# Kernel optimization log

Hardware: AMD Instinct MI355X
Metric: run time of the kernel (lower is better)

## Reference

```python
import jax, jax.numpy as jnp
import numpy as np
from jax import lax

B, N, C, H, M = 256, 2048, 128, 64, 50
NMS_THRESH = 2.0  # forward() calls target_nms(..., 2)
LN_EPS = 1e-5


def setup_inputs() -> dict:
    key = jax.random.key(0)
    ks = jax.random.split(key, 32)
    w = lambda k, shape: jax.random.normal(k, shape, jnp.float32) * 0.02
    gt_idx = jax.random.randint(ks[2], (B,), 0, N)
    inp = {
        "feat_in": jax.random.normal(ks[0], (B, 1, C), jnp.float32),
        "tar_candidate": jax.random.normal(ks[1], (B, N, 2), jnp.float32) * 10.0,
        "mask": jnp.zeros((B, N, 1), jnp.float32),
        "candidate_gt": jax.nn.one_hot(gt_idx, N, dtype=jnp.float32),
        "offset_gt": jax.random.normal(ks[3], (B, 2), jnp.float32),
    }
    Din = C + 2
    # prob_mlp params
    inp.update(p_w1=w(ks[4], (Din, H)), p_b1=jnp.zeros((H,)), p_g1=jnp.ones((H,)), p_be1=jnp.zeros((H,)),
               p_w2=w(ks[5], (H, H)), p_b2=jnp.zeros((H,)), p_g2=jnp.ones((H,)), p_be2=jnp.zeros((H,)),
               p_w3=w(ks[6], (H, 1)), p_b3=jnp.zeros((1,)))
    # offset_mlp params
    inp.update(o_w1=w(ks[7], (Din, H)), o_b1=jnp.zeros((H,)), o_g1=jnp.ones((H,)), o_be1=jnp.zeros((H,)),
               o_w2=w(ks[8], (H, H)), o_g2=jnp.ones((H,)), o_b2=jnp.zeros((H,)), o_be2=jnp.zeros((H,)),
               o_w3=w(ks[9], (H, 2)), o_b3=jnp.zeros((2,)))
    return inp


def _ln(x, g, b):
    mu = jnp.mean(x, axis=-1, keepdims=True)
    var = jnp.mean((x - mu) ** 2, axis=-1, keepdims=True)
    return (x - mu) * lax.rsqrt(var + LN_EPS) * g + b


def _mlp(x, w1, b1, g1, be1, w2, b2, g2, be2, w3, b3):
    h = jax.nn.relu(_ln(x @ w1 + b1, g1, be1))
    h = jax.nn.relu(_ln(h @ w2 + b2, g2, be2))
    return h @ w3 + b3


def _target_nms(targets, threshold):
    # targets: [B, 50, 2] -> [B, 6, 2], sequential dedup per batch row
    def per_batch(t):
        sel0 = t[:6]

        def step(carry, i):
            sel, cnt = carry
            d = jnp.sum((sel - t[i]) ** 2, axis=1)            # [6]
            valid = jnp.arange(6) < cnt
            close = jnp.any((d < threshold) & valid)
            accept = jnp.logical_and(~close, cnt < 6)
            sel = sel.at[cnt].set(jnp.where(accept, t[i], sel[cnt]))
            cnt = cnt + accept.astype(jnp.int32)
            return (sel, cnt), None

        (sel, _), _ = lax.scan(step, (sel0, jnp.int32(1)), jnp.arange(1, M))
        return sel

    return jax.vmap(per_batch)(targets)


def _forward(feat_in, tar_candidate, mask, candidate_gt, offset_gt,
             p_w1, p_b1, p_g1, p_be1, p_w2, p_b2, p_g2, p_be2, p_w3, p_b3,
             o_w1, o_b1, o_g1, o_be1, o_w2, o_b2, o_g2, o_be2, o_w3, o_b3):
    b, n, _ = tar_candidate.shape
    feat_rep = jnp.concatenate(
        [jnp.broadcast_to(feat_in, (b, n, feat_in.shape[-1])), tar_candidate], axis=2)  # [B,N,C+2]

    prob_tensor = _mlp(feat_rep, p_w1, p_b1, p_g1, p_be1, p_w2, p_b2, p_g2, p_be2, p_w3, p_b3)
    prob_tensor = prob_tensor + mask
    tar_candit_prob = jax.nn.softmax(prob_tensor, axis=1)[..., 0]                      # [B,N]

    tar_offset = _mlp(feat_rep, o_w1, o_b1, o_g1, o_be1, o_w2, o_b2, o_g2, o_be2, o_w3, o_b3)  # [B,N,2]

    _, idx = lax.top_k(tar_candit_prob, M)                                             # [B,50]
    idx3 = jnp.repeat(idx[:, :, None], 2, axis=2)
    tar_sel = jnp.take_along_axis(tar_candidate, idx3, axis=1) + jnp.take_along_axis(tar_offset, idx3, axis=1)
    tar_sel = _target_nms(tar_sel, NMS_THRESH)                                         # [B,6,2]

    # loss: BCE(prob, gt) + smooth_l1(offset[gt], offset_gt); gt is one-hot per row
    p = tar_candit_prob
    bce = -jnp.mean(candidate_gt * jnp.clip(jnp.log(p), -100.0)
                    + (1.0 - candidate_gt) * jnp.clip(jnp.log1p(-p), -100.0))
    gt_idx = jnp.argmax(candidate_gt, axis=1)                                          # [B]
    off_pred = tar_offset[jnp.arange(b), gt_idx]                                       # [B,2]
    d = off_pred - offset_gt
    ad = jnp.abs(d)
    sl1 = jnp.mean(jnp.where(ad < 1.0, 0.5 * d * d, ad - 0.5))
    loss = bce + sl1
    return tar_sel, loss


def reference(feat_in, tar_candidate, mask, candidate_gt, offset_gt,
              p_w1, p_b1, p_g1, p_be1, p_w2, p_b2, p_g2, p_be2, p_w3, p_b3,
              o_w1, o_b1, o_g1, o_be1, o_w2, o_b2, o_g2, o_be2, o_w3, o_b3):
    return _forward(feat_in, tar_candidate, mask, candidate_gt, offset_gt,
                    p_w1, p_b1, p_g1, p_be1, p_w2, p_b2, p_g2, p_be2, p_w3, p_b3,
                    o_w1, o_b1, o_g1, o_be1, o_w2, o_b2, o_g2, o_be2, o_w3, o_b3)
```

## Files before the change

### kernel.cpp

```cpp
#include <hip/hip_runtime.h>
#include <hip/hip_bf16.h>
#include <math.h>

#define Bb 256
#define Nn 2048
#define Cc 128
#define Hh 64
#define Mm 50

__global__ __launch_bounds__(128) void k_base(const float* __restrict__ feat,
                                              const float* __restrict__ p_w1,
                                              const float* __restrict__ p_b1,
                                              const float* __restrict__ o_w1,
                                              const float* __restrict__ o_b1,
                                              float* __restrict__ basep,
                                              float* __restrict__ baseo) {
    int b = blockIdx.x, tid = threadIdx.x;
    int k = tid & 63;
    bool lo = tid < 64;
    const float* w1 = lo ? p_w1 : o_w1;
    const float* b1 = lo ? p_b1 : o_b1;
    float* dst = lo ? basep : baseo;
    const float* f = feat + b * Cc;
    float s = b1[k];
    #pragma unroll 8
    for (int c = 0; c < Cc; ++c) s = fmaf(f[c], w1[c * Hh + k], s);
    dst[b * Hh + k] = s;
}

__global__ __launch_bounds__(256, 1) void k_mlp_p(
    const float* __restrict__ cand, const float* __restrict__ basep,
    const float* __restrict__ p_w1, const float* __restrict__ p_g1, const float* __restrict__ p_be1,
    const float* __restrict__ p_w2, const float* __restrict__ p_b2,
    const float* __restrict__ p_g2, const float* __restrict__ p_be2,
    const float* __restrict__ p_w3, const float* __restrict__ p_b3,
    float* __restrict__ logits)
{
    int tid = threadIdx.x;
    int b = blockIdx.x >> 3;
    int n = ((blockIdx.x & 7) << 8) + tid;
    long row = (long)b * Nn + n;
    float cx = cand[row * 2 + 0];
    float cy = cand[row * 2 + 1];
    const float* basev = basep + b * Hh;
    const float* u = p_w1 + 128 * Hh;
    const float* v = p_w1 + 129 * Hh;

    float a[Hh];
    float sum = 0.f, sq = 0.f;
    #pragma unroll
    for (int j = 0; j < Hh; ++j) {
        float t = fmaf(cy, v[j], fmaf(cx, u[j], basev[j]));
        a[j] = t;
        sum += t;
        sq = fmaf(t, t, sq);
    }
    float mu = sum * (1.f / Hh);
    float rstd = rsqrtf(sq * (1.f / Hh) - mu * mu + 1e-5f);
    #pragma unroll
    for (int j = 0; j < Hh; ++j)
        a[j] = fmaxf(fmaf((a[j] - mu) * rstd, p_g1[j], p_be1[j]), 0.f);

    float h[Hh];
    #pragma unroll
    for (int i = 0; i < Hh; ++i) h[i] = 0.f;
    #pragma unroll
    for (int j = 0; j < Hh; ++j) {
        float av = a[j];
        const float* w2r = p_w2 + j * Hh;
        #pragma unroll
        for (int i = 0; i < Hh; ++i) h[i] = fmaf(av, w2r[i], h[i]);
    }
    float sum2 = 0.f, sq2 = 0.f;
    #pragma unroll
    for (int i = 0; i < Hh; ++i) {
        float hv = h[i] + p_b2[i];
        h[i] = hv;
        sum2 += hv;
        sq2 = fmaf(hv, hv, sq2);
    }
    float mu2 = sum2 * (1.f / Hh);
    float rstd2 = rsqrtf(sq2 * (1.f / Hh) - mu2 * mu2 + 1e-5f);

    float lg = p_b3[0];
    #pragma unroll
    for (int i = 0; i < Hh; ++i) {
        float aa = fmaxf(fmaf((h[i] - mu2) * rstd2, p_g2[i], p_be2[i]), 0.f);
        lg = fmaf(aa, p_w3[i], lg);
    }
    logits[row] = lg;
}

__global__ __launch_bounds__(256) void k_post(
    const float* __restrict__ logits, const float* __restrict__ mask,
    const float* __restrict__ gt,
    float* __restrict__ bce_part, int* __restrict__ selidx_g, int* __restrict__ gidx_g)
{
    __shared__ float vals[Nn];
    __shared__ float redf[4];
    __shared__ float wvv[4]; __shared__ int wvi[4];
    __shared__ int   gidx_sh;
    __shared__ int   wini_sh;
    __shared__ int   selidx[Mm];

    int b = blockIdx.x, tid = threadIdx.x;
    int wave = tid >> 6, lane = tid & 63;
    const float* lg = logits + (long)b * Nn;
    const float* mk = mask + (long)b * Nn;

    float xv[8];
    float mx = -1e30f;
    #pragma unroll
    for (int k = 0; k < 8; ++k) {
        int n = tid + k * 256;
        xv[k] = lg[n] + mk[n];
        mx = fmaxf(mx, xv[k]);
    }
    #pragma unroll
    for (int m = 1; m < 64; m <<= 1) mx = fmaxf(mx, __shfl_xor(mx, m));
    if (lane == 0) redf[wave] = mx;
    __syncthreads();
    float m = fmaxf(fmaxf(redf[0], redf[1]), fmaxf(redf[2], redf[3]));
    __syncthreads();

    float ev[8]; float es = 0.f;
    #pragma unroll
    for (int k = 0; k < 8; ++k) { ev[k] = expf(xv[k] - m); es += ev[k]; }
    #pragma unroll
    for (int mm = 1; mm < 64; mm <<= 1) es += __shfl_xor(es, mm);
    if (lane == 0) redf[wave] = es;
    __syncthreads();
    float invZ = 1.f / (((redf[0] + redf[1]) + redf[2]) + redf[3]);

    const float* g = gt + (long)b * Nn;
    float bs = 0.f;
    #pragma unroll
    for (int k = 0; k < 8; ++k) {
        int n = tid + k * 256;
        float pv = ev[k] * invZ;
        vals[n] = pv;
        float gv = g[n];
        float lp = fmaxf(logf(pv), -100.f);
        float l1p = fmaxf(log1pf(-pv), -100.f);
        bs += gv * lp + (1.f - gv) * l1p;
        if (gv > 0.5f) gidx_sh = n;
    }
    #pragma unroll
    for (int mm = 1; mm < 64; mm <<= 1) bs += __shfl_xor(bs, mm);
    if (lane == 0) redf[wave] = bs;
    __syncthreads();
    if (tid == 0) {
        bce_part[b] = ((redf[0] + redf[1]) + redf[2]) + redf[3];
        gidx_g[b] = gidx_sh;
    }

    float bv = -1.f; int bi = 0x7fffffff;
    #pragma unroll
    for (int k = 0; k < 8; ++k) {
        int n = tid + k * 256;
        float v = vals[n];
        if (v > bv) { bv = v; bi = n; }
    }
    for (int it = 0; it < Mm; ++it) {
        float rv = bv; int ri = bi;
        #pragma unroll
        for (int mm = 1; mm < 64; mm <<= 1) {
            float v2 = __shfl_xor(rv, mm); int i2 = __shfl_xor(ri, mm);
            if (v2 > rv || (v2 == rv && i2 < ri)) { rv = v2; ri = i2; }
        }
        if (lane == 0) { wvv[wave] = rv; wvi[wave] = ri; }
        __syncthreads();
        if (tid == 0) {
            float wv = wvv[0]; int wi = wvi[0];
            #pragma unroll
            for (int k = 1; k < 4; ++k) {
                if (wvv[k] > wv || (wvv[k] == wv && wvi[k] < wi)) { wv = wvv[k]; wi = wvi[k]; }
            }
            wini_sh = wi;
            selidx[it] = wi;
        }
        __syncthreads();
        int wi = wini_sh;
        if ((wi & 255) == tid) {
            vals[wi] = -1.f;
            bv = -1.f; bi = 0x7fffffff;
            #pragma unroll
            for (int k = 0; k < 8; ++k) {
                int n = tid + k * 256;
                float v = vals[n];
                if (v > bv) { bv = v; bi = n; }
            }
        }
    }
    if (tid < Mm) selidx_g[b * Mm + tid] = selidx[tid];
}

__device__ __forceinline__ void off_mlp_row(
    long row, const float* __restrict__ cand, const float* __restrict__ basev,
    const float* __restrict__ o_w1, const float* __restrict__ o_g1, const float* __restrict__ o_be1,
    const float* __restrict__ o_w2, const float* __restrict__ o_b2,
    const float* __restrict__ o_g2, const float* __restrict__ o_be2,
    const float* __restrict__ o_w3, const float* __restrict__ o_b3,
    float& o0, float& o1)
{
    float cx = cand[row * 2 + 0];
    float cy = cand[row * 2 + 1];
    const float* u = o_w1 + 128 * Hh;
    const float* v = o_w1 + 129 * Hh;
    float a[Hh];
    float sum = 0.f, sq = 0.f;
    #pragma unroll
    for (int j = 0; j < Hh; ++j) {
        float t = fmaf(cy, v[j], fmaf(cx, u[j], basev[j]));
        a[j] = t;
        sum += t;
        sq = fmaf(t, t, sq);
    }
    float mu = sum * (1.f / Hh);
    float rstd = rsqrtf(sq * (1.f / Hh) - mu * mu + 1e-5f);
    #pragma unroll
    for (int j = 0; j < Hh; ++j)
        a[j] = fmaxf(fmaf((a[j] - mu) * rstd, o_g1[j], o_be1[j]), 0.f);
    float h[Hh];
    #pragma unroll
    for (int i = 0; i < Hh; ++i) h[i] = 0.f;
    #pragma unroll
    for (int j = 0; j < Hh; ++j) {
        float av = a[j];
        const float* w2r = o_w2 + j * Hh;
        #pragma unroll
        for (int i = 0; i < Hh; ++i) h[i] = fmaf(av, w2r[i], h[i]);
    }
    float sum2 = 0.f, sq2 = 0.f;
    #pragma unroll
    for (int i = 0; i < Hh; ++i) {
        float hv = h[i] + o_b2[i];
        h[i] = hv;
        sum2 += hv;
        sq2 = fmaf(hv, hv, sq2);
    }
    float mu2 = sum2 * (1.f / Hh);
    float rstd2 = rsqrtf(sq2 * (1.f / Hh) - mu2 * mu2 + 1e-5f);
    o0 = o_b3[0]; o1 = o_b3[1];
    #pragma unroll
    for (int i = 0; i < Hh; ++i) {
        float aa = fmaxf(fmaf((h[i] - mu2) * rstd2, o_g2[i], o_be2[i]), 0.f);
        o0 = fmaf(aa, o_w3[i * 2 + 0], o0);
        o1 = fmaf(aa, o_w3[i * 2 + 1], o1);
    }
}

__global__ __launch_bounds__(64, 1) void k_off(
    const float* __restrict__ cand, const float* __restrict__ baseo,
    const int* __restrict__ selidx_g, const int* __restrict__ gidx_g,
    const float* __restrict__ off_gt,
    const float* __restrict__ o_w1, const float* __restrict__ o_g1, const float* __restrict__ o_be1,
    const float* __restrict__ o_w2, const float* __restrict__ o_b2,
    const float* __restrict__ o_g2, const float* __restrict__ o_be2,
    const float* __restrict__ o_w3, const float* __restrict__ o_b3,
    float* __restrict__ out, float* __restrict__ sl1_part)
{
    __shared__ float tx[Mm], ty[Mm];
    int b = blockIdx.x, tid = threadIdx.x;
    const float* basev = baseo + b * Hh;

    int idx;
    if (tid < Mm)        idx = selidx_g[b * Mm + tid];
    else if (tid == Mm)  idx = gidx_g[b];
    else                 idx = 0;
    long row = (long)b * Nn + idx;

    float o0, o1;
    off_mlp_row(row, cand, basev, o_w1, o_g1, o_be1, o_w2, o_b2, o_g2, o_be2, o_w3, o_b3, o0, o1);

    if (tid < Mm) {
        tx[tid] = cand[row * 2 + 0] + o0;
        ty[tid] = cand[row * 2 + 1] + o1;
    } else if (tid == Mm) {
        float s1 = 0.f;
        float d0 = o0 - off_gt[b * 2 + 0];
        float ad0 = fabsf(d0);
        s1 += (ad0 < 1.f) ? 0.5f * d0 * d0 : ad0 - 0.5f;
        float d1 = o1 - off_gt[b * 2 + 1];
        float ad1 = fabsf(d1);
        s1 += (ad1 < 1.f) ? 0.5f * d1 * d1 : ad1 - 0.5f;
        sl1_part[b] = s1;
    }
    __syncthreads();
    if (tid == 0) {
        float sx[6], sy[6];
        #pragma unroll
        for (int k = 0; k < 6; ++k) { sx[k] = tx[k]; sy[k] = ty[k]; }
        int cnt = 1;
        for (int i = 1; i < Mm; ++i) {
            bool close = false;
            #pragma unroll
            for (int k = 0; k < 6; ++k) {
                float dx = sx[k] - tx[i], dy = sy[k] - ty[i];
                close = close || ((k < cnt) && (dx * dx + dy * dy < 2.0f));
            }
            if (!close && cnt < 6) { sx[cnt] = tx[i]; sy[cnt] = ty[i]; cnt++; }
        }
        #pragma unroll
        for (int k = 0; k < 6; ++k) {
            out[(b * 6 + k) * 2 + 0] = sx[k];
            out[(b * 6 + k) * 2 + 1] = sy[k];
        }
    }
}

__global__ __launch_bounds__(256) void k_loss(const float* __restrict__ bce_part,
                                              const float* __restrict__ sl1_part,
                                              float* __restrict__ out) {
    __shared__ float redb[4], reds[4];
    int tid = threadIdx.x, wave = tid >> 6, lane = tid & 63;
    float sb = bce_part[tid];
    float ss = sl1_part[tid];
    #pragma unroll
    for (int mm = 1; mm < 64; mm <<= 1) { sb += __shfl_xor(sb, mm); ss += __shfl_xor(ss, mm); }
    if (lane == 0) { redb[wave] = sb; reds[wave] = ss; }
    __syncthreads();
    if (tid == 0) {
        float tb = ((redb[0] + redb[1]) + redb[2]) + redb[3];
        float ts = ((reds[0] + reds[1]) + reds[2]) + reds[3];
        out[0] = -tb / (float)(Bb * Nn) + ts / (float)(Bb * 2);
    }
}

extern "C" void kernel_launch(void* const* d_in, const int* in_sizes, int n_in,
                              void* d_out, int out_size, void* d_ws, size_t ws_size,
                              hipStream_t stream) {
    const float* feat  = (const float*)d_in[0];
    const float* cand  = (const float*)d_in[1];
    const float* mask  = (const float*)d_in[2];
    const float* gt    = (const float*)d_in[3];
    const float* ogt   = (const float*)d_in[4];
    const float* p_w1  = (const float*)d_in[5];
    const float* p_b1  = (const float*)d_in[6];
    const float* p_g1  = (const float*)d_in[7];
    const float* p_be1 = (const float*)d_in[8];
    const float* p_w2  = (const float*)d_in[9];
    const float* p_b2  = (const float*)d_in[10];
    const float* p_g2  = (const float*)d_in[11];
    const float* p_be2 = (const float*)d_in[12];
    const float* p_w3  = (const float*)d_in[13];
    const float* p_b3  = (const float*)d_in[14];
    const float* o_w1  = (const float*)d_in[15];
    const float* o_b1  = (const float*)d_in[16];
    const float* o_g1  = (const float*)d_in[17];
    const float* o_be1 = (const float*)d_in[18];
    const float* o_w2  = (const float*)d_in[19];
    const float* o_g2  = (const float*)d_in[20];
    const float* o_b2  = (const float*)d_in[21];
    const float* o_be2 = (const float*)d_in[22];
    const float* o_w3  = (const float*)d_in[23];
    const float* o_b3  = (const float*)d_in[24];

    float* ws       = (float*)d_ws;
    float* basep    = ws;
    float* baseo    = basep + Bb * Hh;
    float* logits   = baseo + Bb * Hh;
    float* bce_part = logits + (long)Bb * Nn;
    float* sl1_part = bce_part + Bb;
    int*   selidx_g = (int*)(sl1_part + Bb);
    int*   gidx_g   = selidx_g + Bb * Mm;

    float* out = (float*)d_out;

    k_base<<<Bb, 128, 0, stream>>>(feat, p_w1, p_b1, o_w1, o_b1, basep, baseo);
    k_mlp_p<<<Bb * 8, 256, 0, stream>>>(cand, basep,
        p_w1, p_g1, p_be1, p_w2, p_b2, p_g2, p_be2, p_w3, p_b3, logits);
    k_post<<<Bb, 256, 0, stream>>>(logits, mask, gt, bce_part, selidx_g, gidx_g);
    k_off<<<Bb, 64, 0, stream>>>(cand, baseo, selidx_g, gidx_g, ogt,
        o_w1, o_g1, o_be1, o_w2, o_b2, o_g2, o_be2, o_w3, o_b3, out, sl1_part);
    k_loss<<<1, 256, 0, stream>>>(bce_part, sl1_part, out + Bb * 6 * 2);
}
```

Before: 151.9 us.

## Fuse base projection into MLP kernels and stage weights in shared memory

Removes the separate k_base launch. Each k_mlp_p block now computes its batch row's feature projection for the prob MLP, and k_off computes the offset projection itself. k_mlp_p also stages W2 and the packed per-channel parameters into LDS and recomputes the layer-1 activations on the fly instead of holding a 64-entry array, which cuts register pressure and scalar global loads. The cost is redundant projection work: each of the 8 blocks per batch row repeats the 128x64 dot products in a single wave while the other waves wait at the barrier.

Measured after the change: 190.1 us. +25.1%, slower.

```diff
diff --git a/kernel.cpp b/kernel.cpp
--- a/kernel.cpp
+++ b/kernel.cpp
@@ -8,73 +8,72 @@
 #define Hh 64
 #define Mm 50
 
-__global__ __launch_bounds__(128) void k_base(const float* __restrict__ feat,
-                                              const float* __restrict__ p_w1,
-                                              const float* __restrict__ p_b1,
-                                              const float* __restrict__ o_w1,
-                                              const float* __restrict__ o_b1,
-                                              float* __restrict__ basep,
-                                              float* __restrict__ baseo) {
-    int b = blockIdx.x, tid = threadIdx.x;
-    int k = tid & 63;
-    bool lo = tid < 64;
-    const float* w1 = lo ? p_w1 : o_w1;
-    const float* b1 = lo ? p_b1 : o_b1;
-    float* dst = lo ? basep : baseo;
-    const float* f = feat + b * Cc;
-    float s = b1[k];
-    #pragma unroll 8
-    for (int c = 0; c < Cc; ++c) s = fmaf(f[c], w1[c * Hh + k], s);
-    dst[b * Hh + k] = s;
-}
-
 __global__ __launch_bounds__(256, 1) void k_mlp_p(
-    const float* __restrict__ cand, const float* __restrict__ basep,
-    const float* __restrict__ p_w1, const float* __restrict__ p_g1, const float* __restrict__ p_be1,
+    const float* __restrict__ feat, const float* __restrict__ cand,
+    const float* __restrict__ p_w1, const float* __restrict__ p_b1,
+    const float* __restrict__ p_g1, const float* __restrict__ p_be1,
     const float* __restrict__ p_w2, const float* __restrict__ p_b2,
     const float* __restrict__ p_g2, const float* __restrict__ p_be2,
     const float* __restrict__ p_w3, const float* __restrict__ p_b3,
     float* __restrict__ logits)
 {
+    __shared__ float  w2s[Hh * Hh];
+    __shared__ float4 uvb[Hh];
+    __shared__ float2 gb1[Hh];
+    __shared__ float4 pk[Hh];
+
     int tid = threadIdx.x;
     int b = blockIdx.x >> 3;
+
+    const float4* w2v = (const float4*)p_w2;
+    float4* w2sv = (float4*)w2s;
+    #pragma unroll
+    for (int q = 0; q < 4; ++q) w2sv[tid + q * 256] = w2v[tid + q * 256];
+    if (tid < Hh) {
+        gb1[tid] = make_float2(p_g1[tid], p_be1[tid]);
+        pk[tid]  = make_float4(p_g2[tid], p_be2[tid], p_w3[tid], p_b2[tid]);
+        const float* f = feat + b * Cc;
+        float s = p_b1[tid];
+        #pragma unroll 8
+        for (int c = 0; c < Cc; ++c) s = fmaf(f[c], p_w1[c * Hh + tid], s);
+        uvb[tid] = make_float4(p_w1[128 * Hh + tid], p_w1[129 * Hh + tid], s, 0.f);
+    }
+    __syncthreads();
+
     int n = ((blockIdx.x & 7) << 8) + tid;
     long row = (long)b * Nn + n;
     float cx = cand[row * 2 + 0];
     float cy = cand[row * 2 + 1];
-    const float* basev = basep + b * Hh;
-    const float* u = p_w1 + 128 * Hh;
-    const float* v = p_w1 + 129 * Hh;
-
-    float a[Hh];
+
     float sum = 0.f, sq = 0.f;
     #pragma unroll
     for (int j = 0; j < Hh; ++j) {
-        float t = fmaf(cy, v[j], fmaf(cx, u[j], basev[j]));
-        a[j] = t;
+        float4 w = uvb[j];
+        float t = fmaf(cy, w.y, fmaf(cx, w.x, w.z));
         sum += t;
         sq = fmaf(t, t, sq);
     }
     float mu = sum * (1.f / Hh);
     float rstd = rsqrtf(sq * (1.f / Hh) - mu * mu + 1e-5f);
-    #pragma unroll
-    for (int j = 0; j < Hh; ++j)
-        a[j] = fmaxf(fmaf((a[j] - mu) * rstd, p_g1[j], p_be1[j]), 0.f);
 
     float h[Hh];
     #pragma unroll
     for (int i = 0; i < Hh; ++i) h[i] = 0.f;
     #pragma unroll
     for (int j = 0; j < Hh; ++j) {
-        float av = a[j];
-        const float* w2r = p_w2 + j * Hh;
+        float4 w = uvb[j];
+        float t = fmaf(cy, w.y, fmaf(cx, w.x, w.z));
+        float2 g = gb1[j];
+        float av = fmaxf(fmaf((t - mu) * rstd, g.x, g.y), 0.f);
+        const float* w2r = w2s + j * Hh;
         #pragma unroll
         for (int i = 0; i < Hh; ++i) h[i] = fmaf(av, w2r[i], h[i]);
     }
+
     float sum2 = 0.f, sq2 = 0.f;
     #pragma unroll
     for (int i = 0; i < Hh; ++i) {
-        float hv = h[i] + p_b2[i];
+        float hv = h[i] + pk[i].w;
         h[i] = hv;
         sum2 += hv;
         sq2 = fmaf(hv, hv, sq2);
@@ -85,8 +84,9 @@
     float lg = p_b3[0];
     #pragma unroll
     for (int i = 0; i < Hh; ++i) {
-        float aa = fmaxf(fmaf((h[i] - mu2) * rstd2, p_g2[i], p_be2[i]), 0.f);
-        lg = fmaf(aa, p_w3[i], lg);
+        float4 k4 = pk[i];
+        float aa = fmaxf(fmaf((h[i] - mu2) * rstd2, k4.x, k4.y), 0.f);
+        lg = fmaf(aa, k4.z, lg);
     }
     logits[row] = lg;
 }
@@ -196,7 +196,7 @@
 }
 
 __device__ __forceinline__ void off_mlp_row(
-    long row, const float* __restrict__ cand, const float* __restrict__ basev,
+    long row, const float* __restrict__ cand, const float* basev,
     const float* __restrict__ o_w1, const float* __restrict__ o_g1, const float* __restrict__ o_be1,
     const float* __restrict__ o_w2, const float* __restrict__ o_b2,
     const float* __restrict__ o_g2, const float* __restrict__ o_be2,
@@ -251,18 +251,28 @@
 }
 
 __global__ __launch_bounds__(64, 1) void k_off(
-    const float* __restrict__ cand, const float* __restrict__ baseo,
+    const float* __restrict__ cand, const float* __restrict__ feat,
     const int* __restrict__ selidx_g, const int* __restrict__ gidx_g,
     const float* __restrict__ off_gt,
-    const float* __restrict__ o_w1, const float* __restrict__ o_g1, const float* __restrict__ o_be1,
+    const float* __restrict__ o_w1, const float* __restrict__ o_b1,
+    const float* __restrict__ o_g1, const float* __restrict__ o_be1,
     const float* __restrict__ o_w2, const float* __restrict__ o_b2,
     const float* __restrict__ o_g2, const float* __restrict__ o_be2,
     const float* __restrict__ o_w3, const float* __restrict__ o_b3,
     float* __restrict__ out, float* __restrict__ sl1_part)
 {
+    __shared__ float base_s[Hh];
     __shared__ float tx[Mm], ty[Mm];
     int b = blockIdx.x, tid = threadIdx.x;
-    const float* basev = baseo + b * Hh;
+
+    {
+        const float* f = feat + b * Cc;
+        float s = o_b1[tid];
+        #pragma unroll 8
+        for (int c = 0; c < Cc; ++c) s = fmaf(f[c], o_w1[c * Hh + tid], s);
+        base_s[tid] = s;
+    }
+    __syncthreads();
 
     int idx;
     if (tid < Mm)        idx = selidx_g[b * Mm + tid];
@@ -271,7 +281,7 @@
     long row = (long)b * Nn + idx;
 
     float o0, o1;
-    off_mlp_row(row, cand, basev, o_w1, o_g1, o_be1, o_w2, o_b2, o_g2, o_be2, o_w3, o_b3, o0, o1);
+    off_mlp_row(row, cand, base_s, o_w1, o_g1, o_be1, o_w2, o_b2, o_g2, o_be2, o_w3, o_b3, o0, o1);
 
     if (tid < Mm) {
         tx[tid] = cand[row * 2 + 0] + o0;
@@ -357,9 +367,7 @@
     const float* o_b3  = (const float*)d_in[24];
 
     float* ws       = (float*)d_ws;
-    float* basep    = ws;
-    float* baseo    = basep + Bb * Hh;
-    float* logits   = baseo + Bb * Hh;
+    float* logits   = ws;
     float* bce_part = logits + (long)Bb * Nn;
     float* sl1_part = bce_part + Bb;
     int*   selidx_g = (int*)(sl1_part + Bb);
@@ -367,11 +375,10 @@
 
     float* out = (float*)d_out;
 
-    k_base<<<Bb, 128, 0, stream>>>(feat, p_w1, p_b1, o_w1, o_b1, basep, baseo);
-    k_mlp_p<<<Bb * 8, 256, 0, stream>>>(cand, basep,
-        p_w1, p_g1, p_be1, p_w2, p_b2, p_g2, p_be2, p_w3, p_b3, logits);
+    k_mlp_p<<<Bb * 8, 256, 0, stream>>>(feat, cand,
+        p_w1, p_b1, p_g1, p_be1, p_w2, p_b2, p_g2, p_be2, p_w3, p_b3, logits);
     k_post<<<Bb, 256, 0, stream>>>(logits, mask, gt, bce_part, selidx_g, gidx_g);
-    k_off<<<Bb, 64, 0, stream>>>(cand, baseo, selidx_g, gidx_g, ogt,
-        o_w1, o_g1, o_be1, o_w2, o_b2, o_g2, o_be2, o_w3, o_b3, out, sl1_part);
+    k_off<<<Bb, 64, 0, stream>>>(cand, feat, selidx_g, gidx_g, ogt,
+        o_w1, o_b1, o_g1, o_be1, o_w2, o_b2, o_g2, o_be2, o_w3, o_b3, out, sl1_part);
     k_loss<<<1, 256, 0, stream>>>(bce_part, sl1_part, out + Bb * 6 * 2);
 }
```

## Process two rows per thread in prob MLP and one batch row per wave in top-k

Applied to the files above, without the earlier changes.

The probability MLP kernel now has each thread compute two candidate rows, so each weight load from p_w2 is shared across two FMA chains. It recomputes the layer-1 activations instead of storing them, which keeps register use in check. The post kernel maps one batch row to each 64-lane wave instead of one row per 256-thread block. This removes the block-wide __syncthreads reductions from softmax and the 50-step iterative argmax. The trade-off is fewer blocks in both kernels, higher register pressure in the MLP, and four times as much shared memory per block in the post kernel.

Result: slower. 212.3 us (+39.7%).

```diff
diff --git a/kernel.cpp b/kernel.cpp
--- a/kernel.cpp
+++ b/kernel.cpp
@@ -37,58 +37,74 @@
     float* __restrict__ logits)
 {
     int tid = threadIdx.x;
-    int b = blockIdx.x >> 3;
-    int n = ((blockIdx.x & 7) << 8) + tid;
-    long row = (long)b * Nn + n;
-    float cx = cand[row * 2 + 0];
-    float cy = cand[row * 2 + 1];
+    int b = blockIdx.x >> 2;
+    int n0 = ((blockIdx.x & 3) << 9) + tid;
+    long row0 = (long)b * Nn + n0;
+    long row1 = row0 + 256;
+    float2 cA = ((const float2*)cand)[row0];
+    float2 cB = ((const float2*)cand)[row1];
     const float* basev = basep + b * Hh;
     const float* u = p_w1 + 128 * Hh;
     const float* v = p_w1 + 129 * Hh;
 
-    float a[Hh];
-    float sum = 0.f, sq = 0.f;
+    float sumA = 0.f, sqA = 0.f, sumB = 0.f, sqB = 0.f;
     #pragma unroll
     for (int j = 0; j < Hh; ++j) {
-        float t = fmaf(cy, v[j], fmaf(cx, u[j], basev[j]));
-        a[j] = t;
-        sum += t;
-        sq = fmaf(t, t, sq);
-    }
-    float mu = sum * (1.f / Hh);
-    float rstd = rsqrtf(sq * (1.f / Hh) - mu * mu + 1e-5f);
-    #pragma unroll
-    for (int j = 0; j < Hh; ++j)
-        a[j] = fmaxf(fmaf((a[j] - mu) * rstd, p_g1[j], p_be1[j]), 0.f);
-
-    float h[Hh];
-    #pragma unroll
-    for (int i = 0; i < Hh; ++i) h[i] = 0.f;
+        float uj = u[j], vj = v[j], bj = basev[j];
+        float tA = fmaf(cA.y, vj, fmaf(cA.x, uj, bj));
+        float tB = fmaf(cB.y, vj, fmaf(cB.x, uj, bj));
+        sumA += tA; sqA = fmaf(tA, tA, sqA);
+        sumB += tB; sqB = fmaf(tB, tB, sqB);
+    }
+    float muA = sumA * (1.f / Hh);
+    float rstdA = rsqrtf(sqA * (1.f / Hh) - muA * muA + 1e-5f);
+    float muB = sumB * (1.f / Hh);
+    float rstdB = rsqrtf(sqB * (1.f / Hh) - muB * muB + 1e-5f);
+
+    float h0[Hh], h1[Hh];
+    #pragma unroll
+    for (int i = 0; i < Hh; ++i) { h0[i] = 0.f; h1[i] = 0.f; }
     #pragma unroll
     for (int j = 0; j < Hh; ++j) {
-        float av = a[j];
+        float uj = u[j], vj = v[j], bj = basev[j];
+        float g = p_g1[j], be = p_be1[j];
+        float tA = fmaf(cA.y, vj, fmaf(cA.x, uj, bj));
+        float aA = fmaxf(fmaf((tA - muA) * rstdA, g, be), 0.f);
+        float tB = fmaf(cB.y, vj, fmaf(cB.x, uj, bj));
+        float aB = fmaxf(fmaf((tB - muB) * rstdB, g, be), 0.f);
         const float* w2r = p_w2 + j * Hh;
         #pragma unroll
-        for (int i = 0; i < Hh; ++i) h[i] = fmaf(av, w2r[i], h[i]);
-    }
-    float sum2 = 0.f, sq2 = 0.f;
+        for (int i = 0; i < Hh; ++i) {
+            float w = w2r[i];
+            h0[i] = fmaf(aA, w, h0[i]);
+            h1[i] = fmaf(aB, w, h1[i]);
+        }
+    }
+
+    float sum2A = 0.f, sq2A = 0.f, sum2B = 0.f, sq2B = 0.f;
     #pragma unroll
     for (int i = 0; i < Hh; ++i) {
-        float hv = h[i] + p_b2[i];
-        h[i] = hv;
-        sum2 += hv;
-        sq2 = fmaf(hv, hv, sq2);
-    }
-    float mu2 = sum2 * (1.f / Hh);
-    float rstd2 = rsqrtf(sq2 * (1.f / Hh) - mu2 * mu2 + 1e-5f);
-
-    float lg = p_b3[0];
+        float b2 = p_b2[i];
+        float hA = h0[i] + b2; h0[i] = hA; sum2A += hA; sq2A = fmaf(hA, hA, sq2A);
+        float hB = h1[i] + b2; h1[i] = hB; sum2B += hB; sq2B = fmaf(hB, hB, sq2B);
+    }
+    float mu2A = sum2A * (1.f / Hh);
+    float rstd2A = rsqrtf(sq2A * (1.f / Hh) - mu2A * mu2A + 1e-5f);
+    float mu2B = sum2B * (1.f / Hh);
+    float rstd2B = rsqrtf(sq2B * (1.f / Hh) - mu2B * mu2B + 1e-5f);
+
+    float b3 = p_b3[0];
+    float lgA = b3, lgB = b3;
     #pragma unroll
     for (int i = 0; i < Hh; ++i) {
-        float aa = fmaxf(fmaf((h[i] - mu2) * rstd2, p_g2[i], p_be2[i]), 0.f);
-        lg = fmaf(aa, p_w3[i], lg);
-    }
-    logits[row] = lg;
+        float g2 = p_g2[i], be2 = p_be2[i], w3 = p_w3[i];
+        float aA = fmaxf(fmaf((h0[i] - mu2A) * rstd2A, g2, be2), 0.f);
+        lgA = fmaf(aA, w3, lgA);
+        float aB = fmaxf(fmaf((h1[i] - mu2B) * rstd2B, g2, be2), 0.f);
+        lgB = fmaf(aB, w3, lgB);
+    }
+    logits[row0] = lgA;
+    logits[row1] = lgB;
 }
 
 __global__ __launch_bounds__(256) void k_post(
@@ -96,107 +112,81 @@
     const float* __restrict__ gt,
     float* __restrict__ bce_part, int* __restrict__ selidx_g, int* __restrict__ gidx_g)
 {
-    __shared__ float vals[Nn];
-    __shared__ float redf[4];
-    __shared__ float wvv[4]; __shared__ int wvi[4];
-    __shared__ int   gidx_sh;
-    __shared__ int   wini_sh;
-    __shared__ int   selidx[Mm];
-
-    int b = blockIdx.x, tid = threadIdx.x;
-    int wave = tid >> 6, lane = tid & 63;
+    __shared__ float vals[4][Nn];
+    int wave = threadIdx.x >> 6, lane = threadIdx.x & 63;
+    int b = blockIdx.x * 4 + wave;
     const float* lg = logits + (long)b * Nn;
     const float* mk = mask + (long)b * Nn;
-
-    float xv[8];
+    const float* g  = gt + (long)b * Nn;
+    float* vw = vals[wave];
+
+    float xv[32];
     float mx = -1e30f;
     #pragma unroll
-    for (int k = 0; k < 8; ++k) {
-        int n = tid + k * 256;
+    for (int k = 0; k < 32; ++k) {
+        int n = lane + k * 64;
         xv[k] = lg[n] + mk[n];
         mx = fmaxf(mx, xv[k]);
     }
     #pragma unroll
     for (int m = 1; m < 64; m <<= 1) mx = fmaxf(mx, __shfl_xor(mx, m));
-    if (lane == 0) redf[wave] = mx;
-    __syncthreads();
-    float m = fmaxf(fmaxf(redf[0], redf[1]), fmaxf(redf[2], redf[3]));
-    __syncthreads();
-
-    float ev[8]; float es = 0.f;
-    #pragma unroll
-    for (int k = 0; k < 8; ++k) { ev[k] = expf(xv[k] - m); es += ev[k]; }
-    #pragma unroll
-    for (int mm = 1; mm < 64; mm <<= 1) es += __shfl_xor(es, mm);
-    if (lane == 0) redf[wave] = es;
-    __syncthreads();
-    float invZ = 1.f / (((redf[0] + redf[1]) + redf[2]) + redf[3]);
-
-    const float* g = gt + (long)b * Nn;
-    float bs = 0.f;
-    #pragma unroll
-    for (int k = 0; k < 8; ++k) {
-        int n = tid + k * 256;
+
+    float ev[32]; float es = 0.f;
+    #pragma unroll
+    for (int k = 0; k < 32; ++k) { ev[k] = expf(xv[k] - mx); es += ev[k]; }
+    #pragma unroll
+    for (int m = 1; m < 64; m <<= 1) es += __shfl_xor(es, m);
+    float invZ = 1.f / es;
+
+    float bs = 0.f; int gidx = 0x7fffffff;
+    #pragma unroll
+    for (int k = 0; k < 32; ++k) {
+        int n = lane + k * 64;
         float pv = ev[k] * invZ;
-        vals[n] = pv;
+        vw[n] = pv;
         float gv = g[n];
         float lp = fmaxf(logf(pv), -100.f);
         float l1p = fmaxf(log1pf(-pv), -100.f);
         bs += gv * lp + (1.f - gv) * l1p;
-        if (gv > 0.5f) gidx_sh = n;
-    }
-    #pragma unroll
-    for (int mm = 1; mm < 64; mm <<= 1) bs += __shfl_xor(bs, mm);
-    if (lane == 0) redf[wave] = bs;
-    __syncthreads();
-    if (tid == 0) {
-        bce_part[b] = ((redf[0] + redf[1]) + redf[2]) + redf[3];
-        gidx_g[b] = gidx_sh;
-    }
+        if (gv > 0.5f) gidx = min(gidx, n);
+    }
+    #pragma unroll
+    for (int m = 1; m < 64; m <<= 1) {
+        bs += __shfl_xor(bs, m);
+        gidx = min(gidx, __shfl_xor(gidx, m));
+    }
+    if (lane == 0) { bce_part[b] = bs; gidx_g[b] = gidx; }
 
     float bv = -1.f; int bi = 0x7fffffff;
     #pragma unroll
-    for (int k = 0; k < 8; ++k) {
-        int n = tid + k * 256;
-        float v = vals[n];
-        if (v > bv) { bv = v; bi = n; }
+    for (int k = 0; k < 32; ++k) {
+        int n = lane + k * 64;
+        float vv = vw[n];
+        if (vv > bv) { bv = vv; bi = n; }
     }
     for (int it = 0; it < Mm; ++it) {
         float rv = bv; int ri = bi;
         #pragma unroll
-        for (int mm = 1; mm < 64; mm <<= 1) {
-            float v2 = __shfl_xor(rv, mm); int i2 = __shfl_xor(ri, mm);
+        for (int m = 1; m < 64; m <<= 1) {
+            float v2 = __shfl_xor(rv, m); int i2 = __shfl_xor(ri, m);
             if (v2 > rv || (v2 == rv && i2 < ri)) { rv = v2; ri = i2; }
         }
-        if (lane == 0) { wvv[wave] = rv; wvi[wave] = ri; }
-        __syncthreads();
-        if (tid == 0) {
-            float wv = wvv[0]; int wi = wvi[0];
-            #pragma unroll
-            for (int k = 1; k < 4; ++k) {
-                if (wvv[k] > wv || (wvv[k] == wv && wvi[k] < wi)) { wv = wvv[k]; wi = wvi[k]; }
-            }
-            wini_sh = wi;
-            selidx[it] = wi;
-        }
-        __syncthreads();
-        int wi = wini_sh;
-        if ((wi & 255) == tid) {
-            vals[wi] = -1.f;
+        if (lane == 0) selidx_g[b * Mm + it] = ri;
+        if ((ri & 63) == lane) {
+            vw[ri] = -1.f;
             bv = -1.f; bi = 0x7fffffff;
             #pragma unroll
-            for (int k = 0; k < 8; ++k) {
-                int n = tid + k * 256;
-                float v = vals[n];
-                if (v > bv) { bv = v; bi = n; }
+            for (int k = 0; k < 32; ++k) {
+                int n = lane + k * 64;
+                float vv = vw[n];
+                if (vv > bv) { bv = vv; bi = n; }
             }
         }
     }
-    if (tid < Mm) selidx_g[b * Mm + tid] = selidx[tid];
 }
 
 __device__ __forceinline__ void off_mlp_row(
-    long row, const float* __restrict__ cand, const float* __restrict__ basev,
+    long row, const float* __restrict__ cand, const float* basev,
     const float* __restrict__ o_w1, const float* __restrict__ o_g1, const float* __restrict__ o_be1,
     const float* __restrict__ o_w2, const float* __restrict__ o_b2,
     const float* __restrict__ o_g2, const float* __restrict__ o_be2,
@@ -368,9 +358,9 @@
     float* out = (float*)d_out;
 
     k_base<<<Bb, 128, 0, stream>>>(feat, p_w1, p_b1, o_w1, o_b1, basep, baseo);
-    k_mlp_p<<<Bb * 8, 256, 0, stream>>>(cand, basep,
+    k_mlp_p<<<Bb * 4, 256, 0, stream>>>(cand, basep,
         p_w1, p_g1, p_be1, p_w2, p_b2, p_g2, p_be2, p_w3, p_b3, logits);
-    k_post<<<Bb, 256, 0, stream>>>(logits, mask, gt, bce_part, selidx_g, gidx_g);
+    k_post<<<Bb / 4, 256, 0, stream>>>(logits, mask, gt, bce_part, selidx_g, gidx_g);
     k_off<<<Bb, 64, 0, stream>>>(cand, baseo, selidx_g, gidx_g, ogt,
         o_w1, o_g1, o_be1, o_w2, o_b2, o_g2, o_be2, o_w3, o_b3, out, sl1_part);
     k_loss<<<1, 256, 0, stream>>>(bce_part, sl1_part, out + Bb * 6 * 2);
```
